# Kernel tuning notes

Measured on AMD Instinct MI355X. Metric: run time of the kernel, lower is better.

The kernel has to match this reference:

```python
import jax, jax.numpy as jnp
import numpy as np

H = 1024      # hidden_dim
P = 8         # n_paths
K = 2         # top_k
THR = 0.1     # firing_threshold
B = 16384     # batch of tokens


def setup_inputs() -> dict:
    key = jax.random.key(0)
    ks = jax.random.split(key, 8)
    g = lambda k, shape, s=0.02: (jax.random.normal(k, shape, dtype=jnp.float32) * s)
    return {
        "x": jax.random.normal(ks[0], (B, H), dtype=jnp.float32),
        # PathGate: Linear(H, H//2) -> SiLU -> Linear(H//2, P), softmax
        "gate_w1": g(ks[1], (H, H // 2)),
        "gate_b1": jnp.zeros((H // 2,), jnp.float32),
        "gate_w2": g(ks[2], (H // 2, P)),
        "gate_b2": jnp.zeros((P,), jnp.float32),
        # each path: Linear(H,H)+SiLU (stacked over P)
        "path_w": g(ks[3], (P, H, H)),
        "path_b": jnp.zeros((P, H), jnp.float32),
        # out_projs: Linear(H,H,bias=False) per path
        "proj_w": g(ks[4], (P, H, H)),
        # blend scalar parameter (init 0.0 -> alpha = 0.5)
        "blend": jnp.zeros((), jnp.float32),
    }


def reference(x, gate_w1, gate_b1, gate_w2, gate_b2, path_w, path_b, proj_w, blend):
    Bn = x.shape[0]
    # gate probabilities (B, P)
    h = jax.nn.silu(x @ gate_w1 + gate_b1)
    gate = jax.nn.softmax(h @ gate_w2 + gate_b2, axis=-1)

    # hard top-k with firing threshold -> per-token per-path combine weight
    vals, idx = jax.lax.top_k(gate, K)              # (B, K)
    fired = vals > THR                              # (B, K)
    w = jnp.zeros_like(gate).at[jnp.arange(Bn)[:, None], idx].add(
        jnp.where(fired, vals, 0.0))                # (B, P) sparse combine weights

    # path compute (dense over P; same values as masked per-path dispatch)
    path_out = jax.nn.silu(jnp.einsum('bh,phd->pbd', x, path_w) + path_b[:, None, :])
    proj_out = jnp.einsum('pbd,pdo->pbo', path_out, proj_w)   # (P, B, H)

    combined = jnp.einsum('bp,pbo->bo', w, proj_out)          # weighted scatter-combine
    total = w.sum(axis=-1)                                    # (B,)
    has_fired = total > 0
    denom = jnp.where(has_fired, total, 1.0)[:, None]
    combined = jnp.where(has_fired[:, None], combined / denom, x)

    alpha = jax.nn.sigmoid(blend)
    out = alpha * combined + (1.0 - alpha) * x
    return out, gate
```

## Files before the change

kernel.cpp:

```cpp
#include <hip/hip_runtime.h>
#include <hip/hip_bf16.h>
#include <cstdint>

#define B_TOK 16384
#define HDIM  1024
#define HGATE 512
#define NPATH 8
#define THRV  0.1f
#define RESSCALE 512.0f
#define MAXROWS (2 * B_TOK + NPATH * 128)

typedef __bf16 bf16x8 __attribute__((ext_vector_type(8)));
typedef _Float16 f16x8 __attribute__((ext_vector_type(8)));
typedef float  f32x4  __attribute__((ext_vector_type(4)));
typedef unsigned short u16;

__device__ __forceinline__ u16 f2bf(float f) {
    uint32_t u = __float_as_uint(f);
    u += 0x7fff + ((u >> 16) & 1);
    return (u16)(u >> 16);
}
__device__ __forceinline__ float bf2f(u16 v) {
    return __uint_as_float((uint32_t)v << 16);
}
union H16 { _Float16 h; u16 u; };
__device__ __forceinline__ u16 f2h(float f) { H16 t; t.h = (_Float16)f; return t.u; }
__device__ __forceinline__ float h2f(u16 b) { H16 t; t.u = b; return (float)t.h; }
__device__ __forceinline__ float silu_f(float a) {
    return a / (1.0f + expf(-a));
}
__device__ __forceinline__ f32x4 mfma_bf16(bf16x8 a, bf16x8 b, f32x4 c) {
    return __builtin_amdgcn_mfma_f32_16x16x32_bf16(a, b, c, 0, 0, 0);
}
__device__ __forceinline__ f32x4 mfma_f16(f16x8 a, f16x8 b, f32x4 c) {
    return __builtin_amdgcn_mfma_f32_16x16x32_f16(a, b, c, 0, 0, 0);
}
__device__ __forceinline__ void async_lds16(const u16* g, u16* l) {
    __builtin_amdgcn_global_load_lds((const __attribute__((address_space(1))) uint32_t*)g,
                                     (__attribute__((address_space(3))) uint32_t*)l,
                                     16, 0, 0);
}

__global__ void k_convert_x(const float* __restrict__ x, u16* __restrict__ xb,
                            u16* __restrict__ xh, u16* __restrict__ xl) {
    int i = (blockIdx.x * 256 + threadIdx.x) * 4;
    float4 v = *(const float4*)(x + i);
    float vv[4] = {v.x, v.y, v.z, v.w};
    u16 hb[4], hh[4], hl[4];
    #pragma unroll
    for (int c = 0; c < 4; c++) {
        hb[c] = f2bf(vv[c]);
        u16 hi = f2h(vv[c]);
        hh[c] = hi;
        hl[c] = f2h((vv[c] - h2f(hi)) * RESSCALE);
    }
    uint2 ob, oh, ol;
    ob.x = (uint32_t)hb[0] | ((uint32_t)hb[1] << 16);
    ob.y = (uint32_t)hb[2] | ((uint32_t)hb[3] << 16);
    oh.x = (uint32_t)hh[0] | ((uint32_t)hh[1] << 16);
    oh.y = (uint32_t)hh[2] | ((uint32_t)hh[3] << 16);
    ol.x = (uint32_t)hl[0] | ((uint32_t)hl[1] << 16);
    ol.y = (uint32_t)hl[2] | ((uint32_t)hl[3] << 16);
    *(uint2*)(xb + i) = ob;
    *(uint2*)(xh + i) = oh;
    *(uint2*)(xl + i) = ol;
}

__global__ void k_transpose_bf16(const float* __restrict__ W, u16* __restrict__ WT) {
    __shared__ float tile[32][33];
    int p = blockIdx.z;
    const float* Wp = W + (size_t)p * HDIM * HDIM;
    u16* WTp = WT + (size_t)p * HDIM * HDIM;
    int d0 = blockIdx.x * 32, h0 = blockIdx.y * 32;
    int tx = threadIdx.x, ty = threadIdx.y;
    #pragma unroll
    for (int rr = 0; rr < 4; rr++) {
        int r = ty + rr * 8;
        tile[r][tx] = Wp[(size_t)(h0 + r) * HDIM + d0 + tx];
    }
    __syncthreads();
    #pragma unroll
    for (int rr = 0; rr < 4; rr++) {
        int r = ty + rr * 8;
        WTp[(size_t)(d0 + r) * HDIM + h0 + tx] = f2bf(tile[tx][r]);
    }
}

__global__ void k_split_w1(const float* __restrict__ W1, u16* __restrict__ WhT,
                           u16* __restrict__ WlT) {
    __shared__ float tile[32][33];
    int n0 = blockIdx.x * 32, k0 = blockIdx.y * 32;
    int tx = threadIdx.x, ty = threadIdx.y;
    #pragma unroll
    for (int rr = 0; rr < 4; rr++) {
        int r = ty + rr * 8;
        tile[r][tx] = W1[(size_t)(k0 + r) * HGATE + n0 + tx];
    }
    __syncthreads();
    #pragma unroll
    for (int rr = 0; rr < 4; rr++) {
        int r = ty + rr * 8;
        float v = tile[tx][r];
        u16 hi = f2h(v);
        WhT[(size_t)(n0 + r) * HDIM + k0 + tx] = hi;
        WlT[(size_t)(n0 + r) * HDIM + k0 + tx] = f2h((v - h2f(hi)) * RESSCALE);
    }
}

__global__ __launch_bounds__(256) void k_gate_mfma(const u16* __restrict__ Ah,
                                                   const u16* __restrict__ Al,
                                                   const u16* __restrict__ BhT,
                                                   const u16* __restrict__ BlT,
                                                   const float* __restrict__ b1,
                                                   float* __restrict__ Hout) {
    __shared__ __align__(16) u16 smem[32768];
    int t = threadIdx.x;
    int m0 = blockIdx.x * 128, n0 = blockIdx.y * 128;
    int wave = t >> 6, lane = t & 63;
    int quad = lane >> 4, l16 = lane & 15;
    int wr = (wave >> 1) * 64, wc = (wave & 1) * 64;
    f32x4 acc[4][4] = {};
    f32x4 accm[4][4] = {};
    union UV { uint4 u; f16x8 v; };
    int c8 = (t & 3) * 8;
    int rb = t >> 2;
    int wb = wave * 512;

    const u16* pAh0 = Ah + (size_t)(m0 + rb) * HDIM + c8;
    const u16* pAh1 = Ah + (size_t)(m0 + 64 + rb) * HDIM + c8;
    const u16* pAl0 = Al + (size_t)(m0 + rb) * HDIM + c8;
    const u16* pAl1 = Al + (size_t)(m0 + 64 + rb) * HDIM + c8;
    const u16* pBh0 = BhT + (size_t)(n0 + rb) * HDIM + c8;
    const u16* pBh1 = BhT + (size_t)(n0 + 64 + rb) * HDIM + c8;
    const u16* pBl0 = BlT + (size_t)(n0 + rb) * HDIM + c8;
    const u16* pBl1 = BlT + (size_t)(n0 + 64 + rb) * HDIM + c8;

    auto stage = [&](int buf, int kt) {
        u16* s = smem + buf * 16384;
        int ko = kt * 32;
        async_lds16(pAh0 + ko, s + wb);
        async_lds16(pAh1 + ko, s + 2048 + wb);
        async_lds16(pAl0 + ko, s + 4096 + wb);
        async_lds16(pAl1 + ko, s + 6144 + wb);
        async_lds16(pBh0 + ko, s + 8192 + wb);
        async_lds16(pBh1 + ko, s + 10240 + wb);
        async_lds16(pBl0 + ko, s + 12288 + wb);
        async_lds16(pBl1 + ko, s + 14336 + wb);
    };

    stage(0, 0);
    __syncthreads();
    int cur = 0;
    for (int kt = 0; kt < HDIM / 32; kt++) {
        if (kt + 1 < HDIM / 32) stage(cur ^ 1, kt + 1);
        u16* s = smem + cur * 16384;
        u16* lAh = s;
        u16* lAl = s + 4096;
        u16* lBh = s + 8192;
        u16* lBl = s + 12288;
        f16x8 avh[4], avl[4], bvh[4], bvl[4];
        #pragma unroll
        for (int i = 0; i < 4; i++) {
            UV u0; u0.u = *(uint4*)(lAh + ((wr + i * 16 + l16) * 32 + quad * 8));
            avh[i] = u0.v;
            UV u1; u1.u = *(uint4*)(lAl + ((wr + i * 16 + l16) * 32 + quad * 8));
            avl[i] = u1.v;
            UV u2; u2.u = *(uint4*)(lBh + ((wc + i * 16 + l16) * 32 + quad * 8));
            bvh[i] = u2.v;
            UV u3; u3.u = *(uint4*)(lBl + ((wc + i * 16 + l16) * 32 + quad * 8));
            bvl[i] = u3.v;
        }
        #pragma unroll
        for (int i = 0; i < 4; i++)
            #pragma unroll
            for (int j = 0; j < 4; j++) {
                acc[i][j]  = mfma_f16(avh[i], bvh[j], acc[i][j]);
                accm[i][j] = mfma_f16(avh[i], bvl[j], accm[i][j]);
                accm[i][j] = mfma_f16(avl[i], bvh[j], accm[i][j]);
            }
        __syncthreads();
        cur ^= 1;
    }
    const float inv_s = 1.0f / RESSCALE;
    float* smf = (float*)smem;
    #pragma unroll
    for (int half = 0; half < 2; half++) {
        if ((wave >> 1) == half) {
            #pragma unroll
            for (int j = 0; j < 4; j++) {
                float bj = b1[n0 + wc + j * 16 + l16];
                #pragma unroll
                for (int i = 0; i < 4; i++)
                    #pragma unroll
                    for (int r = 0; r < 4; r++) {
                        int rrow = i * 16 + quad * 4 + r;
                        float v = acc[i][j][r] + accm[i][j][r] * inv_s + bj;
                        smf[rrow * 128 + wc + j * 16 + l16] = silu_f(v);
                    }
            }
        }
        __syncthreads();
        #pragma unroll
        for (int it = 0; it < 8; it++) {
            int c = t + it * 256;
            int row = c >> 5, c4 = (c & 31) * 4;
            *(float4*)(Hout + (size_t)(m0 + half * 64 + row) * HGATE + n0 + c4) =
                *(float4*)(smf + c * 4);
        }
        __syncthreads();
    }
}

__global__ __launch_bounds__(256) void k_gate_topk(const float* __restrict__ Hin,
                                                   const float* __restrict__ W2,
                                                   const float* __restrict__ b2,
                                                   float* __restrict__ gate_out,
                                                   float* __restrict__ wnorm,
                                                   int* __restrict__ counts,
                                                   int* __restrict__ tokens,
                                                   uint32_t* __restrict__ slots) {
    __shared__ float w2t[NPATH * HGATE];
    __shared__ int cnt[NPATH];
    __shared__ int baseS[NPATH];
    __shared__ unsigned short tloc[NPATH][64];
    __shared__ uint32_t sloc[64][2];
    int t = threadIdx.x;
    #pragma unroll
    for (int j = 0; j < 16; j++) {
        int i = t + j * 256;
        w2t[(i & 7) * HGATE + (i >> 3)] = W2[i];
    }
    if (t < NPATH) cnt[t] = 0;
    __syncthreads();
    int wave = t >> 6, lane = t & 63;
    #pragma unroll 1
    for (int it = 0; it < 16; it++) {
        int tl = wave * 16 + it;
        int token = blockIdx.x * 64 + tl;
        const float* hrow = Hin + (size_t)token * HGATE;
        float hv[8];
        {
            float4 h0 = *(const float4*)(hrow + lane * 8);
            float4 h1 = *(const float4*)(hrow + lane * 8 + 4);
            hv[0] = h0.x; hv[1] = h0.y; hv[2] = h0.z; hv[3] = h0.w;
            hv[4] = h1.x; hv[5] = h1.y; hv[6] = h1.z; hv[7] = h1.w;
        }
        float logit[8];
        #pragma unroll
        for (int p = 0; p < 8; p++) {
            float s = 0.0f;
            #pragma unroll
            for (int kk = 0; kk < 8; kk++) s += hv[kk] * w2t[p * HGATE + lane * 8 + kk];
            #pragma unroll
            for (int off = 32; off >= 1; off >>= 1) s += __shfl_xor(s, off);
            logit[p] = s + b2[p];
        }
        float mx = logit[0];
        #pragma unroll
        for (int p = 1; p < 8; p++) mx = fmaxf(mx, logit[p]);
        float pr[8], sum = 0.0f;
        #pragma unroll
        for (int p = 0; p < 8; p++) { pr[p] = expf(logit[p] - mx); sum += pr[p]; }
        float inv = 1.0f / sum;
        #pragma unroll
        for (int p = 0; p < 8; p++) pr[p] *= inv;
        int i0 = 0; float v0 = pr[0];
        #pragma unroll
        for (int p = 1; p < 8; p++) { if (pr[p] > v0) { v0 = pr[p]; i0 = p; } }
        int i1 = -1; float v1 = -1.0f;
        #pragma unroll
        for (int p = 0; p < 8; p++) { if (p != i0 && pr[p] > v1) { v1 = pr[p]; i1 = p; } }
        float w0 = (v0 > THRV) ? v0 : 0.0f;
        float w1 = (v1 > THRV) ? v1 : 0.0f;
        float total = w0 + w1;
        float invden = (total > 0.0f) ? (1.0f / total) : 1.0f;
        if (lane < 8) {
            float prl = pr[0];
            #pragma unroll
            for (int p = 1; p < 8; p++) prl = (lane == p) ? pr[p] : prl;
            float wl = 0.0f;
            if (lane == i0) wl = w0 * invden;
            if (lane == i1) wl = w1 * invden;
            gate_out[(size_t)token * 8 + lane] = prl;
            wnorm[(size_t)token * 8 + lane] = wl;
        }
        if (lane == 0) {
            uint32_t e0 = 0xFFFFFFFFu, e1 = 0xFFFFFFFFu;
            if (w0 > 0.0f) {
                int j0 = atomicAdd(&cnt[i0], 1);
                tloc[i0][j0] = (unsigned short)tl;
                e0 = ((uint32_t)i0 << 16) | (uint32_t)j0;
            }
            if (w1 > 0.0f) {
                int j1 = atomicAdd(&cnt[i1], 1);
                tloc[i1][j1] = (unsigned short)tl;
                e1 = ((uint32_t)i1 << 16) | (uint32_t)j1;
            }
            sloc[tl][0] = e0; sloc[tl][1] = e1;
        }
    }
    __syncthreads();
    if (t < NPATH) baseS[t] = atomicAdd(&counts[t], cnt[t]);
    __syncthreads();
    for (int p = 0; p < NPATH; p++) {
        int n = cnt[p], b = baseS[p];
        for (int j = t; j < n; j += 256)
            tokens[p * B_TOK + b + j] = blockIdx.x * 64 + tloc[p][j];
    }
    if (t < 64) {
        #pragma unroll
        for (int s = 0; s < 2; s++) {
            uint32_t e = sloc[t][s];
            if (e != 0xFFFFFFFFu) {
                int p = e >> 16;
                int j = (int)(e & 0xFFFFu) + baseS[p];
                e = ((uint32_t)p << 16) | (uint32_t)j;
            }
            slots[(size_t)(blockIdx.x * 64 + t) * 2 + s] = e;
        }
    }
}

__global__ void k_prefix(const int* __restrict__ counts, int* __restrict__ poffs) {
    if (threadIdx.x == 0) {
        int o = 0; poffs[0] = 0;
        for (int p = 0; p < NPATH; p++) {
            o += ((counts[p] + 127) >> 7) << 7;
            poffs[p + 1] = o;
        }
    }
}

__global__ __launch_bounds__(256) void k_path1(const u16* __restrict__ A,
                                               const u16* __restrict__ WT,
                                               const float* __restrict__ pb,
                                               u16* __restrict__ hid,
                                               const int* __restrict__ counts,
                                               const int* __restrict__ tokens,
                                               const int* __restrict__ poffs) {
    int p = blockIdx.z;
    int count = counts[p];
    int m0 = blockIdx.x * 128;
    if (m0 >= count) return;
    int n0 = blockIdx.y * 128;
    int base = poffs[p];
    const u16* BT = WT + (size_t)p * HDIM * HDIM;
    const float* bias = pb + (size_t)p * HDIM;

    __shared__ __align__(16) u16 smem[16384];
    __shared__ int idx[128];
    int t = threadIdx.x;
    if (t < 128) {
        int j = m0 + t; if (j > count - 1) j = count - 1;
        idx[t] = tokens[p * B_TOK + j];
    }
    __syncthreads();
    int rowA0 = idx[t >> 2], rowA1 = idx[64 + (t >> 2)];
    int wave = t >> 6, lane = t & 63;
    int quad = lane >> 4, l16 = lane & 15;
    int wr = (wave >> 1) * 64, wc = (wave & 1) * 64;
    f32x4 acc[4][4] = {};
    union UV { uint4 u; bf16x8 v; };
    int c8 = (t & 3) * 8;
    int rb = t >> 2;
    int wb = wave * 512;

    const u16* pA0 = A + (size_t)rowA0 * HDIM + c8;
    const u16* pA1 = A + (size_t)rowA1 * HDIM + c8;
    const u16* pB0 = BT + (size_t)(n0 + rb) * HDIM + c8;
    const u16* pB1 = BT + (size_t)(n0 + 64 + rb) * HDIM + c8;

    auto stage = [&](int buf, int kt) {
        u16* s = smem + buf * 8192;
        int ko = kt * 32;
        async_lds16(pA0 + ko, s + wb);
        async_lds16(pA1 + ko, s + 2048 + wb);
        async_lds16(pB0 + ko, s + 4096 + wb);
        async_lds16(pB1 + ko, s + 6144 + wb);
    };

    stage(0, 0);
    __syncthreads();
    int cur = 0;
    for (int kt = 0; kt < HDIM / 32; kt++) {
        if (kt + 1 < HDIM / 32) stage(cur ^ 1, kt + 1);
        u16* lA = smem + cur * 8192;
        u16* lB = lA + 4096;
        bf16x8 av[4], bv[4];
        #pragma unroll
        for (int i = 0; i < 4; i++) {
            UV ua; ua.u = *(uint4*)(lA + ((wr + i * 16 + l16) * 32 + quad * 8));
            av[i] = ua.v;
            UV ub; ub.u = *(uint4*)(lB + ((wc + i * 16 + l16) * 32 + quad * 8));
            bv[i] = ub.v;
        }
        #pragma unroll
        for (int i = 0; i < 4; i++)
            #pragma unroll
            for (int j = 0; j < 4; j++)
                acc[i][j] = mfma_bf16(av[i], bv[j], acc[i][j]);
        __syncthreads();
        cur ^= 1;
    }
    #pragma unroll
    for (int j = 0; j < 4; j++) {
        float bj = bias[n0 + wc + j * 16 + l16];
        #pragma unroll
        for (int i = 0; i < 4; i++)
            #pragma unroll
            for (int r = 0; r < 4; r++) {
                int rrow = wr + i * 16 + quad * 4 + r;
                smem[rrow * 128 + wc + j * 16 + l16] = f2bf(silu_f(acc[i][j][r] + bj));
            }
    }
    __syncthreads();
    #pragma unroll
    for (int it = 0; it < 8; it++) {
        int c = t + it * 256;
        int row = c >> 4, cc = (c & 15) * 8;
        *(uint4*)(hid + (size_t)(base + m0 + row) * HDIM + n0 + cc) = *(uint4*)(smem + c * 8);
    }
}

__global__ __launch_bounds__(256) void k_path2(const u16* __restrict__ hid,
                                               const u16* __restrict__ WT,
                                               const float* __restrict__ wnorm,
                                               u16* __restrict__ pcomp,
                                               const int* __restrict__ counts,
                                               const int* __restrict__ tokens,
                                               const int* __restrict__ poffs) {
    int p = blockIdx.z;
    int count = counts[p];
    int m0 = blockIdx.x * 128;
    if (m0 >= count) return;
    int n0 = blockIdx.y * 128;
    int base = poffs[p];
    const u16* A = hid + (size_t)base * HDIM;
    const u16* BT = WT + (size_t)p * HDIM * HDIM;

    __shared__ __align__(16) u16 smem[16384];
    __shared__ float wv[128];
    int t = threadIdx.x;
    if (t < 128) {
        int j = m0 + t; if (j > count - 1) j = count - 1;
        int tok = tokens[p * B_TOK + j];
        wv[t] = wnorm[(size_t)tok * NPATH + p];
    }
    int wave = t >> 6, lane = t & 63;
    int quad = lane >> 4, l16 = lane & 15;
    int wr = (wave >> 1) * 64, wc = (wave & 1) * 64;
    f32x4 acc[4][4] = {};
    union UV { uint4 u; bf16x8 v; };
    int c8 = (t & 3) * 8;
    int rb = t >> 2;
    int wb = wave * 512;

    const u16* pA0 = A + (size_t)(m0 + rb) * HDIM + c8;
    const u16* pA1 = A + (size_t)(m0 + 64 + rb) * HDIM + c8;
    const u16* pB0 = BT + (size_t)(n0 + rb) * HDIM + c8;
    const u16* pB1 = BT + (size_t)(n0 + 64 + rb) * HDIM + c8;

    auto stage = [&](int buf, int kt) {
        u16* s = smem + buf * 8192;
        int ko = kt * 32;
        async_lds16(pA0 + ko, s + wb);
        async_lds16(pA1 + ko, s + 2048 + wb);
        async_lds16(pB0 + ko, s + 4096 + wb);
        async_lds16(pB1 + ko, s + 6144 + wb);
    };

    stage(0, 0);
    __syncthreads();
    int cur = 0;
    for (int kt = 0; kt < HDIM / 32; kt++) {
        if (kt + 1 < HDIM / 32) stage(cur ^ 1, kt + 1);
        u16* lA = smem + cur * 8192;
        u16* lB = lA + 4096;
        bf16x8 av[4], bv[4];
        #pragma unroll
        for (int i = 0; i < 4; i++) {
            UV ua; ua.u = *(uint4*)(lA + ((wr + i * 16 + l16) * 32 + quad * 8));
            av[i] = ua.v;
            UV ub; ub.u = *(uint4*)(lB + ((wc + i * 16 + l16) * 32 + quad * 8));
            bv[i] = ub.v;
        }
        #pragma unroll
        for (int i = 0; i < 4; i++)
            #pragma unroll
            for (int j = 0; j < 4; j++)
                acc[i][j] = mfma_bf16(av[i], bv[j], acc[i][j]);
        __syncthreads();
        cur ^= 1;
    }
    #pragma unroll
    for (int j = 0; j < 4; j++) {
        #pragma unroll
        for (int i = 0; i < 4; i++)
            #pragma unroll
            for (int r = 0; r < 4; r++) {
                int rrow = wr + i * 16 + quad * 4 + r;
                smem[rrow * 128 + wc + j * 16 + l16] = f2bf(wv[rrow] * acc[i][j][r]);
            }
    }
    __syncthreads();
    #pragma unroll
    for (int it = 0; it < 8; it++) {
        int c = t + it * 256;
        int row = c >> 4, cc = (c & 15) * 8;
        *(uint4*)(pcomp + (size_t)(base + m0 + row) * HDIM + n0 + cc) = *(uint4*)(smem + c * 8);
    }
}

__global__ __launch_bounds__(256) void k_blend2(const float* __restrict__ x,
                                                const u16* __restrict__ pcomp,
                                                const uint32_t* __restrict__ slots,
                                                const int* __restrict__ poffs,
                                                const float* __restrict__ blendp,
                                                float* __restrict__ out) {
    int t = threadIdx.x, wave = t >> 6, lane = t & 63;
    int token = blockIdx.x * 4 + wave;
    float alpha = 1.0f / (1.0f + expf(-blendp[0]));
    float beta = 1.0f - alpha;
    uint32_t s0 = slots[(size_t)token * 2];
    uint32_t s1 = slots[(size_t)token * 2 + 1];
    bool f0 = (s0 != 0xFFFFFFFFu), f1 = (s1 != 0xFFFFFFFFu);
    size_t r0 = 0, r1 = 0;
    if (f0) { int p = s0 >> 16, j = s0 & 0xFFFF; r0 = (size_t)(poffs[p] + j) * HDIM; }
    if (f1) { int p = s1 >> 16, j = s1 & 0xFFFF; r1 = (size_t)(poffs[p] + j) * HDIM; }
    const float* xrow = x + (size_t)token * HDIM;
    float* orow = out + (size_t)token * HDIM;
    #pragma unroll
    for (int c = 0; c < 4; c++) {
        int col = c * 256 + lane * 4;
        float4 xv = *(const float4*)(xrow + col);
        float4 o;
        if (f0) {
            uint2 u0 = *(const uint2*)(pcomp + r0 + col);
            float a0 = bf2f(u0.x & 0xFFFF), a1 = bf2f(u0.x >> 16);
            float a2 = bf2f(u0.y & 0xFFFF), a3 = bf2f(u0.y >> 16);
            if (f1) {
                uint2 u1 = *(const uint2*)(pcomp + r1 + col);
                a0 += bf2f(u1.x & 0xFFFF); a1 += bf2f(u1.x >> 16);
                a2 += bf2f(u1.y & 0xFFFF); a3 += bf2f(u1.y >> 16);
            }
            o.x = alpha * a0 + beta * xv.x;
            o.y = alpha * a1 + beta * xv.y;
            o.z = alpha * a2 + beta * xv.z;
            o.w = alpha * a3 + beta * xv.w;
        } else {
            o = xv;
        }
        *(float4*)(orow + col) = o;
    }
}

extern "C" void kernel_launch(void* const* d_in, const int* in_sizes, int n_in,
                              void* d_out, int out_size, void* d_ws, size_t ws_size,
                              hipStream_t stream) {
    const float* x   = (const float*)d_in[0];
    const float* gw1 = (const float*)d_in[1];
    const float* gb1 = (const float*)d_in[2];
    const float* gw2 = (const float*)d_in[3];
    const float* gb2 = (const float*)d_in[4];
    const float* pw  = (const float*)d_in[5];
    const float* pb  = (const float*)d_in[6];
    const float* prw = (const float*)d_in[7];
    const float* blend = (const float*)d_in[8];
    float* out = (float*)d_out;
    float* gate_out = out + (size_t)B_TOK * HDIM;

    char* w = (char*)d_ws;
    size_t o = 0;
    u16* xb      = (u16*)(w + o);   o += (size_t)B_TOK * HDIM * 2;
    u16* pathWT  = (u16*)(w + o);   o += (size_t)NPATH * HDIM * HDIM * 2;
    u16* projWT  = (u16*)(w + o);   o += (size_t)NPATH * HDIM * HDIM * 2;
    u16* w1hT    = (u16*)(w + o);   o += (size_t)HGATE * HDIM * 2;
    u16* w1lT    = (u16*)(w + o);   o += (size_t)HGATE * HDIM * 2;
    size_t uni = o;
    float* hbuf  = (float*)(w + uni);
    u16* pcomp   = (u16*)(w + uni);
    size_t hbuf_sz  = (size_t)B_TOK * HGATE * 4;
    size_t pcomp_sz = (size_t)MAXROWS * HDIM * 2;
    o += (hbuf_sz > pcomp_sz ? hbuf_sz : pcomp_sz);
    size_t uni2 = o;
    u16* xh16    = (u16*)(w + uni2);
    u16* xl16    = (u16*)(w + uni2 + (size_t)B_TOK * HDIM * 2);
    u16* hid     = (u16*)(w + uni2);
    o += (size_t)MAXROWS * HDIM * 2;
    float* wnorm = (float*)(w + o); o += (size_t)B_TOK * NPATH * 4;
    int* tokens  = (int*)(w + o);   o += (size_t)NPATH * B_TOK * 4;
    uint32_t* slots = (uint32_t*)(w + o); o += (size_t)B_TOK * 2 * 4;
    int* counts  = (int*)(w + o);   o += 64;
    int* poffs   = (int*)(w + o);   o += 64;

    hipMemsetAsync(counts, 0, NPATH * sizeof(int), stream);
    k_convert_x<<<dim3((B_TOK * HDIM) / 1024), dim3(256), 0, stream>>>(x, xb, xh16, xl16);
    k_split_w1<<<dim3(HGATE / 32, HDIM / 32), dim3(32, 8), 0, stream>>>(gw1, w1hT, w1lT);
    k_transpose_bf16<<<dim3(32, 32, 8), dim3(32, 8), 0, stream>>>(pw, pathWT);
    k_transpose_bf16<<<dim3(32, 32, 8), dim3(32, 8), 0, stream>>>(prw, projWT);
    k_gate_mfma<<<dim3(B_TOK / 128, HGATE / 128), dim3(256), 0, stream>>>(
        xh16, xl16, w1hT, w1lT, gb1, hbuf);
    k_gate_topk<<<dim3(B_TOK / 64), dim3(256), 0, stream>>>(hbuf, gw2, gb2, gate_out,
                                                            wnorm, counts, tokens, slots);
    k_prefix<<<dim3(1), dim3(64), 0, stream>>>(counts, poffs);
    k_path1<<<dim3(128, 8, 8), dim3(256), 0, stream>>>(xb, pathWT, pb, hid,
                                                       counts, tokens, poffs);
    k_path2<<<dim3(128, 8, 8), dim3(256), 0, stream>>>(hid, projWT, wnorm, pcomp,
                                                       counts, tokens, poffs);
    k_blend2<<<dim3(B_TOK / 4), dim3(256), 0, stream>>>(x, pcomp, slots, poffs, blend, out);
}
```

Measured before the change: 627.6 us.

## Swizzle LDS tiles and deepen async copy pipeline with vmcnt-based waits

The three MFMA GEMM kernels now XOR-swizzle the 16-byte column chunks in LDS by row, so the fragment reads by different lanes hit different banks. The full __syncthreads after each k-step is replaced by explicit s_waitcnt vmcnt plus s_barrier, so the next stage's global-to-LDS loads can stay in flight while the current one is computed. The two path GEMMs also move to a three-stage ring buffer, raising LDS use from 32 KB to 48 KB per block. The extra LDS may lower occupancy, and the hand-counted vmcnt values must match the number of async loads issued per stage.

```diff
diff --git a/kernel.cpp b/kernel.cpp
--- a/kernel.cpp
+++ b/kernel.cpp
@@ -40,6 +40,15 @@
                                      (__attribute__((address_space(3))) uint32_t*)l,
                                      16, 0, 0);
 }
+
+#define PIPE_WAIT_BARRIER(N)                                             \
+    do {                                                                 \
+        asm volatile("s_waitcnt vmcnt(" #N ")\n\ts_barrier" ::: "memory"); \
+        __builtin_amdgcn_sched_barrier(0);                               \
+    } while (0)
+#define PIPE_BARRIER() asm volatile("s_barrier" ::: "memory")
+
+#define SWZ(r) (((r) >> 1) & 3)
 
 __global__ void k_convert_x(const float* __restrict__ x, u16* __restrict__ xb,
                             u16* __restrict__ xh, u16* __restrict__ xl) {
@@ -122,18 +131,27 @@
     f32x4 acc[4][4] = {};
     f32x4 accm[4][4] = {};
     union UV { uint4 u; f16x8 v; };
-    int c8 = (t & 3) * 8;
     int rb = t >> 2;
+    int cs = ((t & 3) ^ SWZ(rb)) * 8;
     int wb = wave * 512;
 
-    const u16* pAh0 = Ah + (size_t)(m0 + rb) * HDIM + c8;
-    const u16* pAh1 = Ah + (size_t)(m0 + 64 + rb) * HDIM + c8;
-    const u16* pAl0 = Al + (size_t)(m0 + rb) * HDIM + c8;
-    const u16* pAl1 = Al + (size_t)(m0 + 64 + rb) * HDIM + c8;
-    const u16* pBh0 = BhT + (size_t)(n0 + rb) * HDIM + c8;
-    const u16* pBh1 = BhT + (size_t)(n0 + 64 + rb) * HDIM + c8;
-    const u16* pBl0 = BlT + (size_t)(n0 + rb) * HDIM + c8;
-    const u16* pBl1 = BlT + (size_t)(n0 + 64 + rb) * HDIM + c8;
+    int offA[4], offB[4];
+    #pragma unroll
+    for (int i = 0; i < 4; i++) {
+        int rA = wr + i * 16 + l16;
+        offA[i] = rA * 32 + (quad ^ SWZ(rA)) * 8;
+        int rB = wc + i * 16 + l16;
+        offB[i] = rB * 32 + (quad ^ SWZ(rB)) * 8;
+    }
+
+    const u16* pAh0 = Ah + (size_t)(m0 + rb) * HDIM + cs;
+    const u16* pAh1 = Ah + (size_t)(m0 + 64 + rb) * HDIM + cs;
+    const u16* pAl0 = Al + (size_t)(m0 + rb) * HDIM + cs;
+    const u16* pAl1 = Al + (size_t)(m0 + 64 + rb) * HDIM + cs;
+    const u16* pBh0 = BhT + (size_t)(n0 + rb) * HDIM + cs;
+    const u16* pBh1 = BhT + (size_t)(n0 + 64 + rb) * HDIM + cs;
+    const u16* pBl0 = BlT + (size_t)(n0 + rb) * HDIM + cs;
+    const u16* pBl1 = BlT + (size_t)(n0 + 64 + rb) * HDIM + cs;
 
     auto stage = [&](int buf, int kt) {
         u16* s = smem + buf * 16384;
@@ -147,13 +165,8 @@
         async_lds16(pBl0 + ko, s + 12288 + wb);
         async_lds16(pBl1 + ko, s + 14336 + wb);
     };
-
-    stage(0, 0);
-    __syncthreads();
-    int cur = 0;
-    for (int kt = 0; kt < HDIM / 32; kt++) {
-        if (kt + 1 < HDIM / 32) stage(cur ^ 1, kt + 1);
-        u16* s = smem + cur * 16384;
+    auto compute = [&](int buf) {
+        u16* s = smem + buf * 16384;
         u16* lAh = s;
         u16* lAl = s + 4096;
         u16* lBh = s + 8192;
@@ -161,14 +174,10 @@
         f16x8 avh[4], avl[4], bvh[4], bvl[4];
         #pragma unroll
         for (int i = 0; i < 4; i++) {
-            UV u0; u0.u = *(uint4*)(lAh + ((wr + i * 16 + l16) * 32 + quad * 8));
-            avh[i] = u0.v;
-            UV u1; u1.u = *(uint4*)(lAl + ((wr + i * 16 + l16) * 32 + quad * 8));
-            avl[i] = u1.v;
-            UV u2; u2.u = *(uint4*)(lBh + ((wc + i * 16 + l16) * 32 + quad * 8));
-            bvh[i] = u2.v;
-            UV u3; u3.u = *(uint4*)(lBl + ((wc + i * 16 + l16) * 32 + quad * 8));
-            bvl[i] = u3.v;
+            UV u0; u0.u = *(uint4*)(lAh + offA[i]); avh[i] = u0.v;
+            UV u1; u1.u = *(uint4*)(lAl + offA[i]); avl[i] = u1.v;
+            UV u2; u2.u = *(uint4*)(lBh + offB[i]); bvh[i] = u2.v;
+            UV u3; u3.u = *(uint4*)(lBl + offB[i]); bvl[i] = u3.v;
         }
         #pragma unroll
         for (int i = 0; i < 4; i++)
@@ -178,9 +187,19 @@
                 accm[i][j] = mfma_f16(avh[i], bvl[j], accm[i][j]);
                 accm[i][j] = mfma_f16(avl[i], bvh[j], accm[i][j]);
             }
-        __syncthreads();
-        cur ^= 1;
-    }
+    };
+
+    stage(0, 0);
+    for (int kt = 0; kt < 31; kt++) {
+        stage((kt + 1) & 1, kt + 1);
+        PIPE_WAIT_BARRIER(8);
+        compute(kt & 1);
+        PIPE_BARRIER();
+    }
+    PIPE_WAIT_BARRIER(0);
+    compute(1);
+    PIPE_BARRIER();
+
     const float inv_s = 1.0f / RESSCALE;
     float* smf = (float*)smem;
     #pragma unroll
@@ -347,7 +366,7 @@
     const u16* BT = WT + (size_t)p * HDIM * HDIM;
     const float* bias = pb + (size_t)p * HDIM;
 
-    __shared__ __align__(16) u16 smem[16384];
+    __shared__ __align__(16) u16 smem[24576];
     __shared__ int idx[128];
     int t = threadIdx.x;
     if (t < 128) {
@@ -355,20 +374,29 @@
         idx[t] = tokens[p * B_TOK + j];
     }
     __syncthreads();
-    int rowA0 = idx[t >> 2], rowA1 = idx[64 + (t >> 2)];
+    int rb = t >> 2;
+    int rowA0 = idx[rb], rowA1 = idx[64 + rb];
     int wave = t >> 6, lane = t & 63;
     int quad = lane >> 4, l16 = lane & 15;
     int wr = (wave >> 1) * 64, wc = (wave & 1) * 64;
     f32x4 acc[4][4] = {};
     union UV { uint4 u; bf16x8 v; };
-    int c8 = (t & 3) * 8;
-    int rb = t >> 2;
+    int cs = ((t & 3) ^ SWZ(rb)) * 8;
     int wb = wave * 512;
 
-    const u16* pA0 = A + (size_t)rowA0 * HDIM + c8;
-    const u16* pA1 = A + (size_t)rowA1 * HDIM + c8;
-    const u16* pB0 = BT + (size_t)(n0 + rb) * HDIM + c8;
-    const u16* pB1 = BT + (size_t)(n0 + 64 + rb) * HDIM + c8;
+    int offA[4], offB[4];
+    #pragma unroll
+    for (int i = 0; i < 4; i++) {
+        int rA = wr + i * 16 + l16;
+        offA[i] = rA * 32 + (quad ^ SWZ(rA)) * 8;
+        int rB = wc + i * 16 + l16;
+        offB[i] = rB * 32 + (quad ^ SWZ(rB)) * 8;
+    }
+
+    const u16* pA0 = A + (size_t)rowA0 * HDIM + cs;
+    const u16* pA1 = A + (size_t)rowA1 * HDIM + cs;
+    const u16* pB0 = BT + (size_t)(n0 + rb) * HDIM + cs;
+    const u16* pB1 = BT + (size_t)(n0 + 64 + rb) * HDIM + cs;
 
     auto stage = [&](int buf, int kt) {
         u16* s = smem + buf * 8192;
@@ -378,30 +406,36 @@
         async_lds16(pB0 + ko, s + 4096 + wb);
         async_lds16(pB1 + ko, s + 6144 + wb);
     };
-
-    stage(0, 0);
-    __syncthreads();
-    int cur = 0;
-    for (int kt = 0; kt < HDIM / 32; kt++) {
-        if (kt + 1 < HDIM / 32) stage(cur ^ 1, kt + 1);
-        u16* lA = smem + cur * 8192;
+    auto compute = [&](int buf) {
+        u16* lA = smem + buf * 8192;
         u16* lB = lA + 4096;
         bf16x8 av[4], bv[4];
         #pragma unroll
         for (int i = 0; i < 4; i++) {
-            UV ua; ua.u = *(uint4*)(lA + ((wr + i * 16 + l16) * 32 + quad * 8));
-            av[i] = ua.v;
-            UV ub; ub.u = *(uint4*)(lB + ((wc + i * 16 + l16) * 32 + quad * 8));
-            bv[i] = ub.v;
+            UV ua; ua.u = *(uint4*)(lA + offA[i]); av[i] = ua.v;
+            UV ub; ub.u = *(uint4*)(lB + offB[i]); bv[i] = ub.v;
         }
         #pragma unroll
         for (int i = 0; i < 4; i++)
             #pragma unroll
             for (int j = 0; j < 4; j++)
                 acc[i][j] = mfma_bf16(av[i], bv[j], acc[i][j]);
-        __syncthreads();
-        cur ^= 1;
-    }
+    };
+
+    stage(0, 0);
+    stage(1, 1);
+    for (int kt = 0; kt < 30; kt++) {
+        stage((kt + 2) % 3, kt + 2);
+        PIPE_WAIT_BARRIER(8);
+        compute(kt % 3);
+        PIPE_BARRIER();
+    }
+    PIPE_WAIT_BARRIER(4);
+    compute(0);
+    PIPE_WAIT_BARRIER(0);
+    compute(1);
+    PIPE_BARRIER();
+
     #pragma unroll
     for (int j = 0; j < 4; j++) {
         float bj = bias[n0 + wc + j * 16 + l16];
@@ -438,7 +472,7 @@
     const u16* A = hid + (size_t)base * HDIM;
     const u16* BT = WT + (size_t)p * HDIM * HDIM;
 
-    __shared__ __align__(16) u16 smem[16384];
+    __shared__ __align__(16) u16 smem[24576];
     __shared__ float wv[128];
     int t = threadIdx.x;
     if (t < 128) {
@@ -446,19 +480,29 @@
         int tok = tokens[p * B_TOK + j];
         wv[t] = wnorm[(size_t)tok * NPATH + p];
     }
+    __syncthreads();
+    int rb = t >> 2;
     int wave = t >> 6, lane = t & 63;
     int quad = lane >> 4, l16 = lane & 15;
     int wr = (wave >> 1) * 64, wc = (wave & 1) * 64;
     f32x4 acc[4][4] = {};
     union UV { uint4 u; bf16x8 v; };
-    int c8 = (t & 3) * 8;
-    int rb = t >> 2;
+    int cs = ((t & 3) ^ SWZ(rb)) * 8;
     int wb = wave * 512;
 
-    const u16* pA0 = A + (size_t)(m0 + rb) * HDIM + c8;
-    const u16* pA1 = A + (size_t)(m0 + 64 + rb) * HDIM + c8;
-    const u16* pB0 = BT + (size_t)(n0 + rb) * HDIM + c8;
-    const u16* pB1 = BT + (size_t)(n0 + 64 + rb) * HDIM + c8;
+    int offA[4], offB[4];
+    #pragma unroll
+    for (int i = 0; i < 4; i++) {
+        int rA = wr + i * 16 + l16;
+        offA[i] = rA * 32 + (quad ^ SWZ(rA)) * 8;
+        int rB = wc + i * 16 + l16;
+        offB[i] = rB * 32 + (quad ^ SWZ(rB)) * 8;
+    }
+
+    const u16* pA0 = A + (size_t)(m0 + rb) * HDIM + cs;
+    const u16* pA1 = A + (size_t)(m0 + 64 + rb) * HDIM + cs;
+    const u16* pB0 = BT + (size_t)(n0 + rb) * HDIM + cs;
+    const u16* pB1 = BT + (size_t)(n0 + 64 + rb) * HDIM + cs;
 
     auto stage = [&](int buf, int kt) {
         u16* s = smem + buf * 8192;
@@ -468,30 +512,36 @@
         async_lds16(pB0 + ko, s + 4096 + wb);
         async_lds16(pB1 + ko, s + 6144 + wb);
     };
-
-    stage(0, 0);
-    __syncthreads();
-    int cur = 0;
-    for (int kt = 0; kt < HDIM / 32; kt++) {
-        if (kt + 1 < HDIM / 32) stage(cur ^ 1, kt + 1);
-        u16* lA = smem + cur * 8192;
+    auto compute = [&](int buf) {
+        u16* lA = smem + buf * 8192;
         u16* lB = lA + 4096;
         bf16x8 av[4], bv[4];
         #pragma unroll
         for (int i = 0; i < 4; i++) {
-            UV ua; ua.u = *(uint4*)(lA + ((wr + i * 16 + l16) * 32 + quad * 8));
-            av[i] = ua.v;
-            UV ub; ub.u = *(uint4*)(lB + ((wc + i * 16 + l16) * 32 + quad * 8));
-            bv[i] = ub.v;
+            UV ua; ua.u = *(uint4*)(lA + offA[i]); av[i] = ua.v;
+            UV ub; ub.u = *(uint4*)(lB + offB[i]); bv[i] = ub.v;
         }
         #pragma unroll
         for (int i = 0; i < 4; i++)
             #pragma unroll
             for (int j = 0; j < 4; j++)
                 acc[i][j] = mfma_bf16(av[i], bv[j], acc[i][j]);
-        __syncthreads();
-        cur ^= 1;
-    }
+    };
+
+    stage(0, 0);
+    stage(1, 1);
+    for (int kt = 0; kt < 30; kt++) {
+        stage((kt + 2) % 3, kt + 2);
+        PIPE_WAIT_BARRIER(8);
+        compute(kt % 3);
+        PIPE_BARRIER();
+    }
+    PIPE_WAIT_BARRIER(4);
+    compute(0);
+    PIPE_WAIT_BARRIER(0);
+    compute(1);
+    PIPE_BARRIER();
+
     #pragma unroll
     for (int j = 0; j < 4; j++) {
         #pragma unroll
```

Result: faster. 598.7 us (-4.6%).
